# Kernel optimization log

Measured on AMD Instinct MI355X. Metric: run time of the kernel, lower is better.

Reference implementation:

```python
import jax, jax.numpy as jnp
import numpy as np

B, D, H = 4096, 64, 1024  # batch, state dim, hidden width


def setup_inputs() -> dict:
    key = jax.random.key(0)
    ks = jax.random.split(key, 4)
    def w(k, shape, fan_in):
        return (jax.random.normal(k, shape, jnp.float32) / np.float32(np.sqrt(fan_in)))
    return {
        "x": jax.random.normal(ks[0], (B, 1 + D), jnp.float32),
        "W1": w(ks[1], (D, H), D),
        "b1": jnp.zeros((H,), jnp.float32),
        "W2": w(ks[2], (H, H), H),
        "b2": jnp.zeros((H,), jnp.float32),
        "W3": w(ks[3], (H, D), H),
        "b3": jnp.zeros((D,), jnp.float32),
    }


def _mlp(z, W1, b1, W2, b2, W3, b3):
    # tanh MLP vector field: d -> h -> h -> d
    h = jnp.tanh(z @ W1 + b1)
    h = jnp.tanh(h @ W2 + b2)
    return h @ W3 + b3


def reference(x, W1, b1, W2, b2, W3, b3):
    x_in = x[:, 1:]                        # [B, D] state (col 0 is logp channel)
    f = lambda z: _mlp(z, W1, b1, W2, b2, W3, b3)
    x_out = f(x_in)                        # [B, D]

    # Exact Jacobian trace: same math as the torch per-dim autograd.grad loop,
    # expressed as D forward-mode JVPs vmapped over the identity basis.
    eye = jnp.eye(x_in.shape[1], dtype=x.dtype)

    def diag_entry(e):                     # e: [D] basis vector
        _, t = jax.jvp(f, (x_in,), (jnp.broadcast_to(e, x_in.shape),))
        return t @ e                       # [B] = J[:, i, i]

    trJ = jnp.sum(jax.vmap(diag_entry)(eye), axis=0)  # [B]

    out = jnp.concatenate([-trJ[:, None], x_out], axis=1)  # [B, 1+D]
    return out + 0.0 * x  # faithful to `+ 0 * x` in the original
```

## Files before the change

### kernel.cpp

```cpp
#include <hip/hip_runtime.h>
#include <cmath>

typedef unsigned short u16;
typedef __attribute__((ext_vector_type(8))) short s8v;
typedef __attribute__((ext_vector_type(4))) float f4v;
typedef __attribute__((ext_vector_type(16))) float f16v;

__device__ __forceinline__ u16 f2bf(float f) {
    union { float f; unsigned u; } v; v.f = f;
    unsigned r = v.u + 0x7FFFu + ((v.u >> 16) & 1u);
    return (u16)(r >> 16);
}
__device__ __forceinline__ float tanh_fast(float x) {
    float e = __builtin_amdgcn_exp2f(x * 2.88539008177792681f);
    return 1.f - 2.f * __builtin_amdgcn_rcpf(1.f + e);
}
__device__ __forceinline__ int wslot(int row, int c) {
    return ((((c >> 2) << 6) | ((c & 3) << 4) | (row & 15)) ^ c);
}
__device__ __forceinline__ size_t fragoff(int n, int k) {
    return (((size_t)(n >> 5) * 64 + (k >> 4)) * 64 + (n & 31) + (((k >> 3) & 1) << 5)) * 8 + (k & 7);
}

__launch_bounds__(256)
__global__ void cnf_prep(const float* __restrict__ x, const float* __restrict__ W1,
                         const float* __restrict__ W2, const float* __restrict__ W3,
                         u16* __restrict__ W2Tf, u16* __restrict__ VTf,
                         u16* __restrict__ xb, u16* __restrict__ W1T,
                         u16* __restrict__ W3Tf, float* __restrict__ trJ)
{
    __shared__ float w2s[32][33];
    __shared__ __align__(16) float w1s[64][36];
    const int a = blockIdx.x * 32;
    const int b = blockIdx.y * 32;
    const int t = threadIdx.x;

    #pragma unroll
    for (int it = 0; it < 4; ++it) {
        int idx = t + it * 256;
        w2s[idx >> 5][idx & 31] = W2[(a + (idx >> 5)) * 1024 + b + (idx & 31)];
    }
    #pragma unroll
    for (int it = 0; it < 8; ++it) {
        int idx = t + it * 256;
        w1s[idx >> 5][idx & 31] = W1[(idx >> 5) * 1024 + a + (idx & 31)];
    }
    __syncthreads();

    #pragma unroll
    for (int it = 0; it < 4; ++it) {
        int idx = t + it * 256;
        int rr = idx >> 5, cc = idx & 31;
        W2Tf[fragoff(b + rr, a + cc)] = f2bf(w2s[cc][rr]);
    }
    {
        const int q = t >> 3, pg = t & 7;
        const float* w3row = W3 + (b + q) * 64;
        f4v u = f4v{0.f, 0.f, 0.f, 0.f};
        #pragma unroll
        for (int i4 = 0; i4 < 16; ++i4) {
            f4v w3v = *(const f4v*)&w3row[i4 * 4];
            #pragma unroll
            for (int s = 0; s < 4; ++s) {
                f4v wv = *(const f4v*)&w1s[i4 * 4 + s][pg * 4];
                u += w3v[s] * wv;
            }
        }
        #pragma unroll
        for (int j = 0; j < 4; ++j) {
            const int pp = pg * 4 + j;
            VTf[fragoff(b + q, a + pp)] = f2bf(w2s[pp][q] * u[j]);
        }
    }
    {
        int bid = blockIdx.y * 32 + blockIdx.x;
        int e = bid * 256 + t;
        xb[e] = f2bf(x[(e >> 6) * 65 + 1 + (e & 63)]);
    }
    if (blockIdx.y == 0) {
        int pp = t >> 3, i0 = (t & 7) * 8;
        s8v v;
        #pragma unroll
        for (int j = 0; j < 8; ++j) v[j] = (short)f2bf(w1s[i0 + j][pp]);
        *(s8v*)&W1T[(a + pp) * 64 + i0] = v;
        if (t < 128) trJ[blockIdx.x * 128 + t] = 0.f;
    }
    if (blockIdx.y == 1) {
        int idx = blockIdx.x * 256 + t;
        int n = idx & 63, k0 = (idx >> 6) * 8;
        s8v v;
        #pragma unroll
        for (int j = 0; j < 8; ++j) v[j] = (short)f2bf(W3[(k0 + j) * 64 + n]);
        *(s8v*)&W3Tf[fragoff(n, k0)] = v;
    }
}

__launch_bounds__(256)
__global__ void cnf_gemm1(const u16* __restrict__ xb, const u16* __restrict__ W1T,
                          const float* __restrict__ b1,
                          u16* __restrict__ h1, u16* __restrict__ g1)
{
    __shared__ __align__(16) u16 lds[12 * 1024];
    __shared__ __align__(16) u16 hls[128 * 64];
    __shared__ __align__(16) u16 gls[128 * 64];
    const int t = threadIdx.x;
    const int wave = t >> 6, lane = t & 63;
    const int wm = wave >> 1, wn = wave & 1;
    const int g = lane >> 4, lr = lane & 15;
    const int arow0 = blockIdx.x * 128, bcol0 = blockIdx.y * 64;

    #pragma unroll
    for (int i = 0; i < 4; ++i) {
        int ch = t + i * 256, row = ch >> 3, c = ch & 7;
        *(s8v*)&lds[(row >> 4) * 1024 + wslot(row, c) * 8] =
            *(const s8v*)&xb[(arow0 + row) * 64 + c * 8];
    }
    #pragma unroll
    for (int i = 0; i < 2; ++i) {
        int ch = t + i * 256, row = ch >> 3, c = ch & 7;
        *(s8v*)&lds[(8 + (row >> 4)) * 1024 + wslot(row, c) * 8] =
            *(const s8v*)&W1T[(bcol0 + row) * 64 + c * 8];
    }
    __syncthreads();

    f4v acc[4][2];
    #pragma unroll
    for (int mi = 0; mi < 4; ++mi)
        #pragma unroll
        for (int ni = 0; ni < 2; ++ni) acc[mi][ni] = f4v{0.f,0.f,0.f,0.f};

    #pragma unroll
    for (int ks = 0; ks < 2; ++ks) {
        const int lo = (ks * 64 + (lane ^ ((ks * 4 + g) & 7))) * 8;
        s8v af[4], bf[2];
        #pragma unroll
        for (int mi = 0; mi < 4; ++mi) af[mi] = *(const s8v*)&lds[(wm * 4 + mi) * 1024 + lo];
        #pragma unroll
        for (int ni = 0; ni < 2; ++ni) bf[ni] = *(const s8v*)&lds[(8 + wn * 2 + ni) * 1024 + lo];
        #pragma unroll
        for (int mi = 0; mi < 4; ++mi)
            #pragma unroll
            for (int ni = 0; ni < 2; ++ni)
                acc[mi][ni] = __builtin_amdgcn_mfma_f32_16x16x32_bf16(af[mi], bf[ni], acc[mi][ni], 0, 0, 0);
    }

    #pragma unroll
    for (int mi = 0; mi < 4; ++mi) {
        const int rowl = wm * 64 + mi * 16 + g * 4;
        #pragma unroll
        for (int ni = 0; ni < 2; ++ni) {
            const int coll = wn * 32 + ni * 16 + lr;
            const float bv = b1[bcol0 + coll];
            const int cc = coll >> 3, jj = coll & 7;
            #pragma unroll
            for (int r = 0; r < 4; ++r) {
                const int row = rowl + r;
                float h = tanh_fast(acc[mi][ni][r] + bv);
                int idx = row * 64 + ((cc ^ (row & 7)) << 3) + jj;
                hls[idx] = f2bf(h);
                gls[idx] = f2bf(1.f - h * h);
            }
        }
    }
    __syncthreads();

    #pragma unroll
    for (int i = 0; i < 4; ++i) {
        int id = i * 256 + t;
        int row = id >> 3, ch = id & 7;
        int src = row * 64 + ((ch ^ (row & 7)) << 3);
        size_t dst = (size_t)(arow0 + row) * 1024 + bcol0 + ch * 8;
        *(s8v*)&h1[dst] = *(const s8v*)&hls[src];
        *(s8v*)&g1[dst] = *(const s8v*)&gls[src];
    }
}

#define LOADA(dh, dg, ko) \
    do { dh = *(const s8v*)(h1p + (ko)); dg = *(const s8v*)(g1p + (ko)); } while (0)

#define LOADB(B, kkg)                                                          \
    do { _Pragma("unroll")                                                     \
         for (int _ks = 0; _ks < 2; ++_ks) {                                   \
             size_t _o = (((size_t)(ntb + wn) * 64 + (kkg) * 2 + _ks) * 64 + lane) * 8; \
             B[_ks*2 + 0] = *(const s8v*)&W2Tf[_o];                            \
             B[_ks*2 + 1] = *(const s8v*)&VTf[_o];                             \
         } } while (0)

#define WRITEA(sh, sg, bb)                                                     \
    do { u16* _wb = &lds[bb][0];                                               \
         *(s8v*)&_wb[sdst] = sh; *(s8v*)&_wb[4096 + sdst] = sg; } while (0)

#define MIDBODY(kt, AwH, AwG, AlH, AlG, Bc, Bn)                                \
    {                                                                          \
        if ((kt) < 30) { const int _ko = ((kt) + 2) * 32; LOADA(AlH, AlG, _ko); } \
        if ((kt) < 31) { WRITEA(AwH, AwG, ((kt) + 1) & 1); LOADB(Bn, (kt) + 1); } \
        const u16* buf = &lds[(kt) & 1][0];                                    \
        _Pragma("unroll")                                                      \
        for (int ks = 0; ks < 2; ++ks) {                                       \
            const int lp = (lane ^ ((lane >> 5) << 2) ^ (ks << 1)) * 8;        \
            s8v a1[2], a2[2];                                                  \
            _Pragma("unroll")                                                  \
            for (int mt = 0; mt < 2; ++mt) {                                   \
                const int R = (wrt * 2 + mt) * 2 + ks;                         \
                a1[mt] = *(const s8v*)&buf[R * 512 + lp];                      \
                a2[mt] = *(const s8v*)&buf[4096 + R * 512 + lp];               \
            }                                                                  \
            _Pragma("unroll")                                                  \
            for (int mt = 0; mt < 2; ++mt) {                                   \
                acc1[mt] = __builtin_amdgcn_mfma_f32_32x32x16_bf16(a1[mt], Bc[ks*2+0], acc1[mt], 0, 0, 0); \
                acc2[mt] = __builtin_amdgcn_mfma_f32_32x32x16_bf16(a2[mt], Bc[ks*2+1], acc2[mt], 0, 0, 0); \
            }                                                                  \
        }                                                                      \
        __syncthreads();                                                       \
    }

__launch_bounds__(512, 1)
__global__ void cnf_mid(const u16* __restrict__ h1, const u16* __restrict__ g1,
                        const u16* __restrict__ W2Tf, const u16* __restrict__ VTf,
                        const float* __restrict__ b2,
                        u16* __restrict__ h2f, float* __restrict__ trJ)
{
    __shared__ __align__(16) u16 lds[2][8192];

    const int t = threadIdx.x;
    const int wave = t >> 6, lane = t & 63;
    const int wrt = wave & 1;
    const int wn  = wave >> 1;
    const int arow0 = blockIdx.x * 128;
    const int ntb = blockIdx.y * 4;

    const int row = t >> 2, c = t & 3;
    const int R0 = (row >> 5) * 2 + (c >> 1);
    const int L0 = (row & 31) + ((c & 1) << 5);
    const int sdst = (R0 * 64 + (L0 ^ ((L0 >> 5) << 2) ^ ((R0 & 1) << 1))) * 8;
    const u16* h1p = h1 + (size_t)(arow0 + row) * 1024 + c * 8;
    const u16* g1p = g1 + (size_t)(arow0 + row) * 1024 + c * 8;

    f16v acc1[2], acc2[2];
    #pragma unroll
    for (int mt = 0; mt < 2; ++mt)
        #pragma unroll
        for (int r = 0; r < 16; ++r) { acc1[mt][r] = 0.f; acc2[mt][r] = 0.f; }

    s8v ahA, agA, ahB, agB;
    s8v bA[4], bB[4];

    LOADA(ahA, agA, 0);
    WRITEA(ahA, agA, 0);
    LOADA(ahB, agB, 32);
    LOADB(bA, 0);
    __syncthreads();

    for (int kt2 = 0; kt2 < 16; ++kt2) {
        const int kt = kt2 * 2;
        MIDBODY(kt,     ahB, agB, ahA, agA, bA, bB);
        MIDBODY(kt + 1, ahA, agA, ahB, agB, bB, bA);
    }

    const int l31 = lane & 31, lh = lane >> 5;
    #pragma unroll
    for (int mt = 0; mt < 2; ++mt) {
        const int rt = (arow0 >> 5) + wrt * 2 + mt;
        const int q0 = (ntb + wn) * 32;
        const float bv = b2[q0 + l31];
        const size_t hb = (((size_t)rt * 64 + ((q0 + l31) >> 4)) * 64
                           + (((l31 >> 3) & 1) << 5)) * 8 + (l31 & 7) + lh * 32;
        float tr[16];
        #pragma unroll
        for (int r = 0; r < 16; ++r) {
            float hh = tanh_fast(acc1[mt][r] + bv);
            float gg = 1.f - hh * hh;
            h2f[hb + ((r & 3) + ((r >> 2) << 3)) * 8] = f2bf(hh);
            tr[r] = acc2[mt][r] * gg;
        }
        #pragma unroll
        for (int off = 1; off < 32; off <<= 1)
            #pragma unroll
            for (int r = 0; r < 16; ++r) tr[r] += __shfl_xor(tr[r], off);
        if (l31 == 0) {
            const int rowb = arow0 + (wrt * 2 + mt) * 32 + lh * 4;
            #pragma unroll
            for (int r = 0; r < 16; ++r)
                atomicAdd(&trJ[rowb + (r & 3) + ((r >> 2) << 3)], tr[r]);
        }
    }
}

__launch_bounds__(256)
__global__ void cnf_out(const u16* __restrict__ h2f, const u16* __restrict__ W3Tf,
                        const float* __restrict__ b3, const float* __restrict__ trJ,
                        float* __restrict__ out)
{
    __shared__ float red[4][32][64];
    const int t = threadIdx.x;
    const int wave = t >> 6, lane = t & 63;
    const int rt = blockIdx.x;

    f16v acc[2];
    #pragma unroll
    for (int ni = 0; ni < 2; ++ni)
        #pragma unroll
        for (int r = 0; r < 16; ++r) acc[ni][r] = 0.f;

    #pragma unroll
    for (int kki = 0; kki < 16; ++kki) {
        const int kk = wave * 16 + kki;
        s8v af = *(const s8v*)&h2f[(((size_t)rt * 64 + kk) * 64 + lane) * 8];
        #pragma unroll
        for (int ni = 0; ni < 2; ++ni) {
            s8v bf = *(const s8v*)&W3Tf[(((size_t)ni * 64 + kk) * 64 + lane) * 8];
            acc[ni] = __builtin_amdgcn_mfma_f32_32x32x16_bf16(af, bf, acc[ni], 0, 0, 0);
        }
    }
    const int l31 = lane & 31, lh = lane >> 5;
    #pragma unroll
    for (int ni = 0; ni < 2; ++ni)
        #pragma unroll
        for (int r = 0; r < 16; ++r)
            red[wave][(r & 3) + ((r >> 2) << 3) + lh * 4][ni * 32 + l31] = acc[ni][r];
    __syncthreads();

    #pragma unroll
    for (int i = 0; i < 8; ++i) {
        int o = t * 8 + i;
        int row = o >> 6, col = o & 63;
        float s = red[0][row][col] + red[1][row][col] + red[2][row][col] + red[3][row][col] + b3[col];
        out[(size_t)(rt * 32 + row) * 65 + 1 + col] = s;
    }
    if (t < 32) out[(size_t)(rt * 32 + t) * 65] = -trJ[rt * 32 + t];
}

extern "C" void kernel_launch(void* const* d_in, const int* in_sizes, int n_in,
                              void* d_out, int out_size, void* d_ws, size_t ws_size,
                              hipStream_t stream) {
    const float* x  = (const float*)d_in[0];
    const float* W1 = (const float*)d_in[1];
    const float* b1 = (const float*)d_in[2];
    const float* W2 = (const float*)d_in[3];
    const float* b2 = (const float*)d_in[4];
    const float* W3 = (const float*)d_in[5];
    const float* b3 = (const float*)d_in[6];
    float* out = (float*)d_out;

    char* ws = (char*)d_ws;
    u16*   h1b = (u16*)(ws);
    u16*   g1b = (u16*)(ws + (size_t)( 8u << 20));
    u16*   h2f = (u16*)(ws + (size_t)(16u << 20));
    u16*   W2T = (u16*)(ws + (size_t)(24u << 20));
    u16*   VTb = (u16*)(ws + (size_t)(26u << 20));
    float* trJ = (float*)(ws + (size_t)(28u << 20));
    u16*   xbb = (u16*)(ws + (size_t)(28u << 20) + 65536);
    u16*   W1T = (u16*)(ws + (size_t)(28u << 20) + 65536 + 524288);
    u16*   W3T = (u16*)(ws + (size_t)(28u << 20) + 65536 + 524288 + 131072);

    cnf_prep <<<dim3(32, 32), 256, 0, stream>>>(x, W1, W2, W3, W2T, VTb, xbb, W1T, W3T, trJ);
    cnf_gemm1<<<dim3(32, 16), 256, 0, stream>>>(xbb, W1T, b1, h1b, g1b);
    cnf_mid  <<<dim3(32, 8),  512, 0, stream>>>(h1b, g1b, W2T, VTb, b2, h2f, trJ);
    cnf_out  <<<128,          256, 0, stream>>>(h2f, W3T, b3, trJ, out);
}
```

Before: 55.49 us.

## Hoist LDS reads before prefetch in mid GEMM, remap blocks, split output kernel

In the mid GEMM loop body, all LDS A-fragment reads now happen before the global prefetch and LDS write for the next tile, so the MFMAs can overlap the memory traffic. The mid kernel launches as a 1D grid, with the low block-id bits picking the N tile, so blocks that share the same A rows run together and may get better L2 reuse. The output kernel is split across two column halves, doubling its block count to raise parallelism in that small kernel. Holding A fragments for both k-steps raises register pressure.

```diff
diff --git a/kernel.cpp b/kernel.cpp
--- a/kernel.cpp
+++ b/kernel.cpp
@@ -192,25 +192,27 @@
 
 #define MIDBODY(kt, AwH, AwG, AlH, AlG, Bc, Bn)                                \
     {                                                                          \
-        if ((kt) < 30) { const int _ko = ((kt) + 2) * 32; LOADA(AlH, AlG, _ko); } \
-        if ((kt) < 31) { WRITEA(AwH, AwG, ((kt) + 1) & 1); LOADB(Bn, (kt) + 1); } \
         const u16* buf = &lds[(kt) & 1][0];                                    \
+        s8v a1[2][2], a2[2][2];                                                \
         _Pragma("unroll")                                                      \
         for (int ks = 0; ks < 2; ++ks) {                                       \
             const int lp = (lane ^ ((lane >> 5) << 2) ^ (ks << 1)) * 8;        \
-            s8v a1[2], a2[2];                                                  \
             _Pragma("unroll")                                                  \
             for (int mt = 0; mt < 2; ++mt) {                                   \
                 const int R = (wrt * 2 + mt) * 2 + ks;                         \
-                a1[mt] = *(const s8v*)&buf[R * 512 + lp];                      \
-                a2[mt] = *(const s8v*)&buf[4096 + R * 512 + lp];               \
+                a1[ks][mt] = *(const s8v*)&buf[R * 512 + lp];                  \
+                a2[ks][mt] = *(const s8v*)&buf[4096 + R * 512 + lp];           \
             }                                                                  \
+        }                                                                      \
+        if ((kt) < 30) { const int _ko = ((kt) + 2) * 32; LOADA(AlH, AlG, _ko); } \
+        if ((kt) < 31) { WRITEA(AwH, AwG, ((kt) + 1) & 1); LOADB(Bn, (kt) + 1); } \
+        _Pragma("unroll")                                                      \
+        for (int ks = 0; ks < 2; ++ks)                                         \
             _Pragma("unroll")                                                  \
             for (int mt = 0; mt < 2; ++mt) {                                   \
-                acc1[mt] = __builtin_amdgcn_mfma_f32_32x32x16_bf16(a1[mt], Bc[ks*2+0], acc1[mt], 0, 0, 0); \
-                acc2[mt] = __builtin_amdgcn_mfma_f32_32x32x16_bf16(a2[mt], Bc[ks*2+1], acc2[mt], 0, 0, 0); \
+                acc1[mt] = __builtin_amdgcn_mfma_f32_32x32x16_bf16(a1[ks][mt], Bc[ks*2+0], acc1[mt], 0, 0, 0); \
+                acc2[mt] = __builtin_amdgcn_mfma_f32_32x32x16_bf16(a2[ks][mt], Bc[ks*2+1], acc2[mt], 0, 0, 0); \
             }                                                                  \
-        }                                                                      \
         __syncthreads();                                                       \
     }
 
@@ -226,8 +228,11 @@
     const int wave = t >> 6, lane = t & 63;
     const int wrt = wave & 1;
     const int wn  = wave >> 1;
-    const int arow0 = blockIdx.x * 128;
-    const int ntb = blockIdx.y * 4;
+    const int bid = blockIdx.x;
+    const int bx  = bid >> 3;
+    const int by  = bid & 7;
+    const int arow0 = bx * 128;
+    const int ntb = by * 4;
 
     const int row = t >> 2, c = t & 3;
     const int R0 = (row >> 5) * 2 + (c >> 1);
@@ -291,43 +296,38 @@
                         const float* __restrict__ b3, const float* __restrict__ trJ,
                         float* __restrict__ out)
 {
-    __shared__ float red[4][32][64];
+    __shared__ float red[4][32][32];
     const int t = threadIdx.x;
     const int wave = t >> 6, lane = t & 63;
     const int rt = blockIdx.x;
-
-    f16v acc[2];
-    #pragma unroll
-    for (int ni = 0; ni < 2; ++ni)
-        #pragma unroll
-        for (int r = 0; r < 16; ++r) acc[ni][r] = 0.f;
+    const int nb = blockIdx.y;
+
+    f16v acc;
+    #pragma unroll
+    for (int r = 0; r < 16; ++r) acc[r] = 0.f;
 
     #pragma unroll
     for (int kki = 0; kki < 16; ++kki) {
         const int kk = wave * 16 + kki;
         s8v af = *(const s8v*)&h2f[(((size_t)rt * 64 + kk) * 64 + lane) * 8];
-        #pragma unroll
-        for (int ni = 0; ni < 2; ++ni) {
-            s8v bf = *(const s8v*)&W3Tf[(((size_t)ni * 64 + kk) * 64 + lane) * 8];
-            acc[ni] = __builtin_amdgcn_mfma_f32_32x32x16_bf16(af, bf, acc[ni], 0, 0, 0);
-        }
+        s8v bf = *(const s8v*)&W3Tf[(((size_t)nb * 64 + kk) * 64 + lane) * 8];
+        acc = __builtin_amdgcn_mfma_f32_32x32x16_bf16(af, bf, acc, 0, 0, 0);
     }
     const int l31 = lane & 31, lh = lane >> 5;
     #pragma unroll
-    for (int ni = 0; ni < 2; ++ni)
-        #pragma unroll
-        for (int r = 0; r < 16; ++r)
-            red[wave][(r & 3) + ((r >> 2) << 3) + lh * 4][ni * 32 + l31] = acc[ni][r];
-    __syncthreads();
-
-    #pragma unroll
-    for (int i = 0; i < 8; ++i) {
-        int o = t * 8 + i;
-        int row = o >> 6, col = o & 63;
-        float s = red[0][row][col] + red[1][row][col] + red[2][row][col] + red[3][row][col] + b3[col];
-        out[(size_t)(rt * 32 + row) * 65 + 1 + col] = s;
-    }
-    if (t < 32) out[(size_t)(rt * 32 + t) * 65] = -trJ[rt * 32 + t];
+    for (int r = 0; r < 16; ++r)
+        red[wave][(r & 3) + ((r >> 2) << 3) + lh * 4][l31] = acc[r];
+    __syncthreads();
+
+    #pragma unroll
+    for (int i = 0; i < 4; ++i) {
+        int o = t + i * 256;
+        int row = o >> 5, col = o & 31;
+        float s = red[0][row][col] + red[1][row][col] + red[2][row][col]
+                + red[3][row][col] + b3[nb * 32 + col];
+        out[(size_t)(rt * 32 + row) * 65 + 1 + nb * 32 + col] = s;
+    }
+    if (nb == 0 && t < 32) out[(size_t)(rt * 32 + t) * 65] = -trJ[rt * 32 + t];
 }
 
 extern "C" void kernel_launch(void* const* d_in, const int* in_sizes, int n_in,
@@ -355,6 +355,6 @@
 
     cnf_prep <<<dim3(32, 32), 256, 0, stream>>>(x, W1, W2, W3, W2T, VTb, xbb, W1T, W3T, trJ);
     cnf_gemm1<<<dim3(32, 16), 256, 0, stream>>>(xbb, W1T, b1, h1b, g1b);
-    cnf_mid  <<<dim3(32, 8),  512, 0, stream>>>(h1b, g1b, W2T, VTb, b2, h2f, trJ);
-    cnf_out  <<<128,          256, 0, stream>>>(h2f, W3T, b3, trJ, out);
-}
+    cnf_mid  <<<256,          512, 0, stream>>>(h1b, g1b, W2T, VTb, b2, h2f, trJ);
+    cnf_out  <<<dim3(128, 2), 256, 0, stream>>>(h2f, W3T, b3, trJ, out);
+}
```

Measured after the change: 58.83 us. +6.0%, slower.
